# Optimization experiments

Measured on AMD Instinct MI355X. Metric: run time of the kernel, lower is better.

Reference implementation:

```python
import jax, jax.numpy as jnp
import numpy as np

N_NODES = 50000
N_RAND_EDGES = 1_600_000
IN_FEATS = 512
HIDDEN = 256
NUM_CLASSES = 64


def setup_inputs() -> dict:
    key = jax.random.key(0)
    ks = jax.random.split(key, 6)
    src = jax.random.randint(ks[0], (N_RAND_EDGES,), 0, N_NODES, dtype=jnp.int32)
    dst = jax.random.randint(ks[1], (N_RAND_EDGES,), 0, N_NODES, dtype=jnp.int32)
    # dgl.add_self_loop(g): append (i, i) for every node
    loop = jnp.arange(N_NODES, dtype=jnp.int32)
    src = jnp.concatenate([src, loop])
    dst = jnp.concatenate([dst, loop])
    features = jax.random.normal(ks[2], (N_NODES, IN_FEATS), dtype=jnp.float32)
    W_conv = jax.random.normal(ks[3], (IN_FEATS, HIDDEN), dtype=jnp.float32) * (1.0 / np.sqrt(IN_FEATS))
    b_conv = jnp.zeros((HIDDEN,), dtype=jnp.float32)
    W2 = jax.random.normal(ks[4], (HIDDEN, NUM_CLASSES), dtype=jnp.float32) * (1.0 / np.sqrt(HIDDEN))
    b2 = jnp.zeros((NUM_CLASSES,), dtype=jnp.float32)
    return {"features": features, "W_conv": W_conv, "b_conv": b_conv,
            "W2": W2, "b2": b2, "src": src, "dst": dst}


def reference(features, W_conv, b_conv, W2, b2, src, dst):
    N = features.shape[0]
    ones = jnp.ones(src.shape[0], dtype=features.dtype)
    # symmetric ('both') normalization as in DGL GraphConv; self-loops guarantee deg >= 1
    deg_out = jax.ops.segment_sum(ones, src, num_segments=N)
    deg_in = jax.ops.segment_sum(ones, dst, num_segments=N)
    norm_src = jax.lax.rsqrt(deg_out)[:, None]  # [N, 1]
    norm_dst = jax.lax.rsqrt(deg_in)[:, None]
    # in_feats > hidden -> DGL multiplies by the weight before aggregating
    h = (features @ W_conv) * norm_src            # [N, H]
    agg = jax.ops.segment_sum(h[src], dst, num_segments=N)  # sparse SpMM: gather + scatter-add
    x = jax.nn.relu(agg * norm_dst + b_conv)      # [N, H]
    # dropout: identity in eval mode (deterministic reference)
    logits = x @ W2 + b2                          # [N, C]
    return jax.nn.log_softmax(logits, axis=1)
```

## Files before the change

kernel.cpp:

```cpp
#include <hip/hip_runtime.h>

typedef unsigned short u16;
typedef unsigned int u32;
typedef __attribute__((ext_vector_type(4))) float f32x4;
typedef __attribute__((ext_vector_type(8))) short s16x8;
typedef __attribute__((ext_vector_type(4))) unsigned short u16x4;
typedef __attribute__((ext_vector_type(8))) unsigned short u16x8;

#define IN_FEATS 512
#define HIDDEN   256
#define NCLS     64
#define NB       128
#define QBINS    12500
#define EPT      13

#define H8_CLIP  2.5f
#define H8_INV   (127.0f / H8_CLIP)
#define H8_SCALE (H8_CLIP / 127.0f)

static __device__ inline u16 f2bf(float f) {
    unsigned int u = __builtin_bit_cast(unsigned int, f);
    unsigned int r = (u + 0x7FFFu + ((u >> 16) & 1u)) >> 16;
    return (u16)r;
}
static __device__ inline float bf2f(u16 u) {
    unsigned int x = ((unsigned int)u) << 16;
    return __builtin_bit_cast(float, x);
}


__launch_bounds__(1024)
__global__ void khist(const int* __restrict__ src, const int* __restrict__ dst,
                      u16* __restrict__ P, int E, int N) {
    __shared__ int bins[QBINS];
    const int b = blockIdx.x;
    const int t = threadIdx.x;
    const int lo = (int)((long)b * E / NB);
    const int hi = (int)((long)(b + 1) * E / NB);

    int se[EPT], de[EPT];
#pragma unroll
    for (int p = 0; p < EPT; p++) {
        int e = lo + t + p * 1024;
        se[p] = 0; de[p] = 0;
        if (e < hi) { se[p] = src[e]; de[p] = dst[e]; }
    }

#pragma unroll 1
    for (int q = 0; q < 4; q++) {
        const int base = q * QBINS;
        __syncthreads();
        for (int j = t; j < QBINS; j += 1024) bins[j] = 0;
        __syncthreads();
#pragma unroll
        for (int p = 0; p < EPT; p++) {
            int e = lo + t + p * 1024;
            if (e < hi) {
                unsigned rs = (unsigned)(se[p] - base), rd = (unsigned)(de[p] - base);
                if (rs < (unsigned)QBINS) atomicAdd(&bins[rs], 1);
                if (rd < (unsigned)QBINS) atomicAdd(&bins[rd], 0x10000);
            }
        }
        for (int e = lo + t + EPT * 1024; e < hi; e += 1024) {
            int s = src[e], d = dst[e];
            unsigned rs = (unsigned)(s - base), rd = (unsigned)(d - base);
            if (rs < (unsigned)QBINS) atomicAdd(&bins[rs], 1);
            if (rd < (unsigned)QBINS) atomicAdd(&bins[rd], 0x10000);
        }
        __syncthreads();
        for (int j = t; j < QBINS; j += 1024) {
            u32 v = (u32)bins[j];
            P[(size_t)b * 50000 + base + j] = (u16)((v & 0xffu) | ((v >> 8) & 0xff00u));
        }
    }
}

__global__ void kred(u16* __restrict__ P, int* __restrict__ deg_in,
                     float* __restrict__ ns, float* __restrict__ nd, int N) {
    int j = blockIdx.x * blockDim.x + threadIdx.x;
    if (j >= N) return;
    u32 so = 0, si = 0;
#pragma unroll 4
    for (int b = 0; b < NB; b++) {
        u32 v = P[(size_t)b * 50000 + j];
        P[(size_t)b * 50000 + j] = (u16)si;
        so += v & 0xffu;
        si += v >> 8;
    }
    deg_in[j] = (int)si;
    ns[j] = rsqrtf((float)so);
    nd[j] = rsqrtf((float)si);
}

__launch_bounds__(256)
__global__ void kscanA(const int* __restrict__ deg, int* __restrict__ rowptr,
                       int* __restrict__ bsum, int N) {
    __shared__ int wsum[4];
    const int b = blockIdx.x, t = threadIdx.x;
    const int lane = t & 63, wave = t >> 6;
    const int j = b * 256 + t;
    int v = (j < N) ? deg[j] : 0;
    int s = v;
#pragma unroll
    for (int off = 1; off < 64; off <<= 1) {
        int u = __shfl_up(s, off);
        if (lane >= off) s += u;
    }
    if (lane == 63) wsum[wave] = s;
    __syncthreads();
    int woff = 0;
#pragma unroll
    for (int w = 0; w < 4; w++) woff += (w < wave) ? wsum[w] : 0;
    if (j < N) rowptr[j] = woff + s - v;
    if (t == 255) bsum[b] = woff + s;
}

__launch_bounds__(256)
__global__ void kscanB(int* __restrict__ rowptr, const int* __restrict__ bsum,
                       int N, int nblk, int E) {
    __shared__ int wsum[4];
    const int b = blockIdx.x, t = threadIdx.x;
    const int lane = t & 63, wave = t >> 6;
    int v = (t < b && t < nblk) ? bsum[t] : 0;
#pragma unroll
    for (int off = 32; off; off >>= 1) v += __shfl_xor(v, off);
    if (lane == 0) wsum[wave] = v;
    __syncthreads();
    int offsum = wsum[0] + wsum[1] + wsum[2] + wsum[3];
    int j = b * 256 + t;
    if (j < N) rowptr[j] += offsum;
    if (b == 0 && t == 0) rowptr[N] = E;
}

__launch_bounds__(1024)
__global__ void kscat(const int* __restrict__ src, const int* __restrict__ dst,
                      const int* __restrict__ rowptr, const u16* __restrict__ P,
                      int* __restrict__ csc, int E, int N) {
    __shared__ int cur[QBINS];
    const int b = blockIdx.x;
    const int t = threadIdx.x;
    const int lo = (int)((long)b * E / NB);
    const int hi = (int)((long)(b + 1) * E / NB);

    int se[EPT], de[EPT];
#pragma unroll
    for (int p = 0; p < EPT; p++) {
        int e = lo + t + p * 1024;
        se[p] = 0; de[p] = 0;
        if (e < hi) { se[p] = src[e]; de[p] = dst[e]; }
    }

#pragma unroll 1
    for (int q = 0; q < 4; q++) {
        const int base = q * QBINS;
        __syncthreads();
        for (int j = t; j < QBINS; j += 1024) {
            int node = base + j;
            cur[j] = (node < N) ? rowptr[node] + (int)P[(size_t)b * 50000 + node] : 0;
        }
        __syncthreads();
#pragma unroll
        for (int p = 0; p < EPT; p++) {
            int e = lo + t + p * 1024;
            if (e < hi) {
                unsigned rd = (unsigned)(de[p] - base);
                if (rd < (unsigned)QBINS) {
                    int pos = atomicAdd(&cur[rd], 1);
                    csc[pos] = se[p] << 8;
                }
            }
        }
        for (int e = lo + t + EPT * 1024; e < hi; e += 1024) {
            int d = dst[e];
            unsigned rd = (unsigned)(d - base);
            if (rd < (unsigned)QBINS) {
                int pos = atomicAdd(&cur[rd], 1);
                csc[pos] = src[e] << 8;
            }
        }
    }
}


__global__ void k_wt(const float* __restrict__ W, u16* __restrict__ Wt) {
    int i = blockIdx.x * blockDim.x + threadIdx.x;
    if (i < IN_FEATS * HIDDEN) {
        int k = i >> 8, n = i & 255;
        Wt[n * IN_FEATS + k] = f2bf(W[i]);
    }
}

__global__ void k_w2t(const float* __restrict__ W2, u16* __restrict__ W2t) {
    int i = blockIdx.x * blockDim.x + threadIdx.x;
    if (i < HIDDEN * NCLS) {
        int k = i >> 6, n = i & 63;
        W2t[n * HIDDEN + k] = f2bf(W2[i]);
    }
}

__global__ void k_zrow(signed char* __restrict__ h8, int N) {
    ((int*)(h8 + (size_t)N * HIDDEN))[threadIdx.x] = 0;
}


static __device__ inline s16x8 ld_frag(const u16* p) {
    u16x4 lo = *(const u16x4*)p;
    u16x4 hi = *(const u16x4*)(p + 4);
    s16x8 r;
    r[0] = (short)lo.x; r[1] = (short)lo.y; r[2] = (short)lo.z; r[3] = (short)lo.w;
    r[4] = (short)hi.x; r[5] = (short)hi.y; r[6] = (short)hi.z; r[7] = (short)hi.w;
    return r;
}

__launch_bounds__(512)
__global__ void k_gemm1(const float* __restrict__ feat, const u16* __restrict__ Wt,
                        const float* __restrict__ norm_src, signed char* __restrict__ h8, int N) {
    __shared__ __align__(16) u16 At[128][40];
    __shared__ __align__(16) u16 Bt[256][40];
    const int t = threadIdx.x;
    const int lane = t & 63;
    const int wave = t >> 6;
    const int wm = wave & 1;
    const int wn = wave >> 1;
    const int m0 = blockIdx.x * 128;
    const int l15 = lane & 15;
    const int l4 = lane >> 4;

    f32x4 acc[4][4] = {};

    for (int kk = 0; kk < IN_FEATS; kk += 32) {
        __syncthreads();
#pragma unroll
        for (int rnd = 0; rnd < 2; rnd++) {
            int slot = t + rnd * 512;
            int r = slot >> 3, q = slot & 7;
            int gr = m0 + r;
            float4 v = make_float4(0.f, 0.f, 0.f, 0.f);
            if (gr < N) v = *(const float4*)&feat[(size_t)gr * IN_FEATS + kk + q * 4];
            u16x4 p;
            p.x = f2bf(v.x); p.y = f2bf(v.y); p.z = f2bf(v.z); p.w = f2bf(v.w);
            *(u16x4*)&At[r][q * 4] = p;
        }
#pragma unroll
        for (int rnd = 0; rnd < 2; rnd++) {
            int slot = t + rnd * 512;
            int r = slot >> 2, q = slot & 3;
            u16x4 w0 = *(const u16x4*)&Wt[(size_t)r * IN_FEATS + kk + q * 8];
            u16x4 w1 = *(const u16x4*)&Wt[(size_t)r * IN_FEATS + kk + q * 8 + 4];
            *(u16x4*)&Bt[r][q * 8] = w0;
            *(u16x4*)&Bt[r][q * 8 + 4] = w1;
        }
        __syncthreads();

        s16x8 a[4], b[4];
#pragma unroll
        for (int mi = 0; mi < 4; mi++) a[mi] = ld_frag(&At[wm * 64 + mi * 16 + l15][l4 * 8]);
#pragma unroll
        for (int ni = 0; ni < 4; ni++) b[ni] = ld_frag(&Bt[wn * 64 + ni * 16 + l15][l4 * 8]);
#pragma unroll
        for (int mi = 0; mi < 4; mi++)
#pragma unroll
            for (int ni = 0; ni < 4; ni++)
                acc[mi][ni] = __builtin_amdgcn_mfma_f32_16x16x32_bf16(a[mi], b[ni], acc[mi][ni], 0, 0, 0);
    }

#pragma unroll
    for (int mi = 0; mi < 4; mi++) {
#pragma unroll
        for (int q = 0; q < 4; q++) {
            int row = m0 + wm * 64 + mi * 16 + l4 * 4 + q;
            if (row < N) {
                float nsv = norm_src[row] * H8_INV;
#pragma unroll
                for (int ni = 0; ni < 4; ni++) {
                    int col = wn * 64 + ni * 16 + l15;
                    int v = (int)rintf(acc[mi][ni][q] * nsv);
                    v = max(-127, min(127, v));
                    h8[(size_t)row * HIDDEN + col] = (signed char)v;
                }
            }
        }
    }
}

__launch_bounds__(256)
__global__ void k_spmm(const signed char* __restrict__ h8, const int* __restrict__ rowptr,
                       const int* __restrict__ csc, const float* __restrict__ nd,
                       const float* __restrict__ bconv, u16* __restrict__ x, int N) {
    const int t = threadIdx.x;
    const int lane = t & 63;
    const int half = lane >> 5;
    const int hl = lane & 31;
    const int ZOFF = N * HIDDEN;
    const int gw = (blockIdx.x * blockDim.x + t) >> 6;
    const int nw = (gridDim.x * blockDim.x) >> 6;
    const int npair = (N + 1) >> 1;

    for (int pair = gw; pair < npair; pair += nw) {
        int node = pair * 2 + half;
        bool valid = node < N;
        int start = 0, deg = 0;
        if (valid) { start = rowptr[node]; deg = rowptr[node + 1] - start; }
        int maxdeg = max(deg, __shfl_xor(deg, 32));
        int a0 = 0, a1 = 0, a2 = 0, a3 = 0, a4 = 0, a5 = 0, a6 = 0, a7 = 0;

        for (int base = 0; base < maxdeg; base += 32) {
            int ev = ZOFF;
            if (base + hl < deg) ev = csc[start + base + hl];
            int cntmax = min(32, maxdeg - base);
            int i = 0;
            for (; i + 4 <= cntmax; i += 4) {
                int sb = (half << 5) + i;
                int o0 = __shfl(ev, sb);
                int o1 = __shfl(ev, sb + 1);
                int o2 = __shfl(ev, sb + 2);
                int o3 = __shfl(ev, sb + 3);
                int2 w0 = *(const int2*)&h8[o0 + hl * 8];
                int2 w1 = *(const int2*)&h8[o1 + hl * 8];
                int2 w2 = *(const int2*)&h8[o2 + hl * 8];
                int2 w3 = *(const int2*)&h8[o3 + hl * 8];
                a0 += ((w0.x << 24) >> 24) + ((w1.x << 24) >> 24) + ((w2.x << 24) >> 24) + ((w3.x << 24) >> 24);
                a1 += ((w0.x << 16) >> 24) + ((w1.x << 16) >> 24) + ((w2.x << 16) >> 24) + ((w3.x << 16) >> 24);
                a2 += ((w0.x << 8) >> 24) + ((w1.x << 8) >> 24) + ((w2.x << 8) >> 24) + ((w3.x << 8) >> 24);
                a3 += (w0.x >> 24) + (w1.x >> 24) + (w2.x >> 24) + (w3.x >> 24);
                a4 += ((w0.y << 24) >> 24) + ((w1.y << 24) >> 24) + ((w2.y << 24) >> 24) + ((w3.y << 24) >> 24);
                a5 += ((w0.y << 16) >> 24) + ((w1.y << 16) >> 24) + ((w2.y << 16) >> 24) + ((w3.y << 16) >> 24);
                a6 += ((w0.y << 8) >> 24) + ((w1.y << 8) >> 24) + ((w2.y << 8) >> 24) + ((w3.y << 8) >> 24);
                a7 += (w0.y >> 24) + (w1.y >> 24) + (w2.y >> 24) + (w3.y >> 24);
            }
            for (; i < cntmax; i++) {
                int o = __shfl(ev, (half << 5) + i);
                int2 w = *(const int2*)&h8[o + hl * 8];
                a0 += (w.x << 24) >> 24;
                a1 += (w.x << 16) >> 24;
                a2 += (w.x << 8) >> 24;
                a3 += w.x >> 24;
                a4 += (w.y << 24) >> 24;
                a5 += (w.y << 16) >> 24;
                a6 += (w.y << 8) >> 24;
                a7 += w.y >> 24;
            }
        }

        if (valid) {
            float scnd = nd[node] * H8_SCALE;
            float4 ba = *(const float4*)&bconv[hl * 8];
            float4 bb = *(const float4*)&bconv[hl * 8 + 4];
            u16x8 o;
            o[0] = f2bf(fmaxf((float)a0 * scnd + ba.x, 0.f));
            o[1] = f2bf(fmaxf((float)a1 * scnd + ba.y, 0.f));
            o[2] = f2bf(fmaxf((float)a2 * scnd + ba.z, 0.f));
            o[3] = f2bf(fmaxf((float)a3 * scnd + ba.w, 0.f));
            o[4] = f2bf(fmaxf((float)a4 * scnd + bb.x, 0.f));
            o[5] = f2bf(fmaxf((float)a5 * scnd + bb.y, 0.f));
            o[6] = f2bf(fmaxf((float)a6 * scnd + bb.z, 0.f));
            o[7] = f2bf(fmaxf((float)a7 * scnd + bb.w, 0.f));
            *(u16x8*)&x[(size_t)node * HIDDEN + hl * 8] = o;
        }
    }
}

__launch_bounds__(256)
__global__ void k_gemm2(const u16* __restrict__ x, const u16* __restrict__ W2t,
                        const float* __restrict__ b2, float* __restrict__ out, int N) {
    __shared__ __align__(16) u16 Bs[NCLS][HIDDEN + 8];
    const int t = threadIdx.x;
    for (int i = t; i < NCLS * HIDDEN / 8; i += 256) {
        int idx = i * 8;
        int n = idx >> 8, k = idx & 255;
        *(u16x8*)&Bs[n][k] = *(const u16x8*)&W2t[n * HIDDEN + k];
    }
    __syncthreads();

    const int lane = t & 63;
    const int wave = t >> 6;
    const int l15 = lane & 15;
    const int l4 = lane >> 4;
    const int r0 = blockIdx.x * 128 + wave * 32;

    float bb[4];
#pragma unroll
    for (int ni = 0; ni < 4; ni++) bb[ni] = b2[ni * 16 + l15];

    f32x4 acc[2][4] = {};
#pragma unroll
    for (int kk = 0; kk < HIDDEN; kk += 32) {
        s16x8 b[4];
#pragma unroll
        for (int ni = 0; ni < 4; ni++) b[ni] = ld_frag(&Bs[ni * 16 + l15][kk + l4 * 8]);
#pragma unroll
        for (int mi = 0; mi < 2; mi++) {
            int row = r0 + mi * 16 + l15;
            s16x8 a = {};
            if (row < N) a = ld_frag(&x[(size_t)row * HIDDEN + kk + l4 * 8]);
#pragma unroll
            for (int ni = 0; ni < 4; ni++)
                acc[mi][ni] = __builtin_amdgcn_mfma_f32_16x16x32_bf16(a, b[ni], acc[mi][ni], 0, 0, 0);
        }
    }

#pragma unroll
    for (int mi = 0; mi < 2; mi++) {
#pragma unroll
        for (int q = 0; q < 4; q++) {
            int row = r0 + mi * 16 + l4 * 4 + q;
            float v0 = acc[mi][0][q] + bb[0];
            float v1 = acc[mi][1][q] + bb[1];
            float v2 = acc[mi][2][q] + bb[2];
            float v3 = acc[mi][3][q] + bb[3];
            float m = fmaxf(fmaxf(v0, v1), fmaxf(v2, v3));
#pragma unroll
            for (int off = 1; off < 16; off <<= 1) m = fmaxf(m, __shfl_xor(m, off));
            float s = __expf(v0 - m) + __expf(v1 - m) + __expf(v2 - m) + __expf(v3 - m);
#pragma unroll
            for (int off = 1; off < 16; off <<= 1) s += __shfl_xor(s, off);
            float lg = m + __logf(s);
            if (row < N) {
                out[(size_t)row * NCLS + 0 * 16 + l15] = v0 - lg;
                out[(size_t)row * NCLS + 1 * 16 + l15] = v1 - lg;
                out[(size_t)row * NCLS + 2 * 16 + l15] = v2 - lg;
                out[(size_t)row * NCLS + 3 * 16 + l15] = v3 - lg;
            }
        }
    }
}


extern "C" void kernel_launch(void* const* d_in, const int* in_sizes, int n_in,
                              void* d_out, int out_size, void* d_ws, size_t ws_size,
                              hipStream_t stream) {
    const float* feat = (const float*)d_in[0];
    const float* Wc   = (const float*)d_in[1];
    const float* bc   = (const float*)d_in[2];
    const float* W2   = (const float*)d_in[3];
    const float* b2   = (const float*)d_in[4];
    const int*   src  = (const int*)d_in[5];
    const int*   dst  = (const int*)d_in[6];
    const int N = in_sizes[0] / IN_FEATS;
    const int E = in_sizes[5];
    float* out = (float*)d_out;

    char* ws = (char*)d_ws;
    size_t off = 0;
    auto alloc = [&](size_t b) {
        char* p = ws + off;
        off = (off + b + 255) & ~(size_t)255;
        return p;
    };
    signed char* h8 = (signed char*)alloc((size_t)(N + 1) * HIDDEN);
    u16* x      = (u16*)alloc((size_t)N * HIDDEN * 2);
    u16* Wt     = (u16*)alloc((size_t)IN_FEATS * HIDDEN * 2);
    u16* W2t    = (u16*)alloc((size_t)HIDDEN * NCLS * 2);
    int* deg_in = (int*)alloc((size_t)N * 4);
    int* rowptr = (int*)alloc((size_t)(N + 1) * 4);
    int* bsum   = (int*)alloc((size_t)256 * 4);
    float* ns   = (float*)alloc((size_t)N * 4);
    float* nd   = (float*)alloc((size_t)N * 4);
    int* csc    = (int*)alloc((size_t)E * 4);
    u16* P      = (u16*)alloc((size_t)NB * 50000 * 2);

    const int nblk = (N + 255) / 256;

    khist<<<dim3(NB), dim3(1024), 0, stream>>>(src, dst, P, E, N);
    kred<<<dim3((N + 255) / 256), dim3(256), 0, stream>>>(P, deg_in, ns, nd, N);
    kscanA<<<dim3(nblk), dim3(256), 0, stream>>>(deg_in, rowptr, bsum, N);
    kscanB<<<dim3(nblk), dim3(256), 0, stream>>>(rowptr, bsum, N, nblk, E);
    kscat<<<dim3(NB), dim3(1024), 0, stream>>>(src, dst, rowptr, P, csc, E, N);
    k_wt<<<dim3((IN_FEATS * HIDDEN + 255) / 256), dim3(256), 0, stream>>>(Wc, Wt);
    k_w2t<<<dim3((HIDDEN * NCLS + 255) / 256), dim3(256), 0, stream>>>(W2, W2t);
    k_zrow<<<dim3(1), dim3(64), 0, stream>>>(h8, N);
    k_gemm1<<<dim3((N + 127) / 128), dim3(512), 0, stream>>>(feat, Wt, ns, h8, N);
    k_spmm<<<dim3(2048), dim3(256), 0, stream>>>(h8, rowptr, csc, nd, bc, x, N);
    k_gemm2<<<dim3((N + 127) / 128), dim3(256), 0, stream>>>(x, W2t, b2, out, N);
}
```

Before: 172.9 us.

## Fuse degree reduction into scan, merge prep kernels, load GEMM1 weights directly

Merges the per-node degree reduction into the first scan kernel, so the deg_in array and one launch go away. Combines the two weight-transpose kernels and the zero-row kernel into one prep launch. In GEMM1, the B fragments are now read straight from global/L2 memory instead of being staged through shared memory, which frees LDS and removes the staging stores. The trade-off is more uncoalesced global reads of Wt per wave, with no data reuse across waves through LDS.

New measurement: 180.9 us. 4.7% more time.

```diff
diff --git a/kernel.cpp b/kernel.cpp
--- a/kernel.cpp
+++ b/kernel.cpp
@@ -22,10 +22,6 @@
     unsigned int u = __builtin_bit_cast(unsigned int, f);
     unsigned int r = (u + 0x7FFFu + ((u >> 16) & 1u)) >> 16;
     return (u16)r;
-}
-static __device__ inline float bf2f(u16 u) {
-    unsigned int x = ((unsigned int)u) << 16;
-    return __builtin_bit_cast(float, x);
 }
 
 
@@ -75,31 +71,27 @@
     }
 }
 
-__global__ void kred(u16* __restrict__ P, int* __restrict__ deg_in,
-                     float* __restrict__ ns, float* __restrict__ nd, int N) {
-    int j = blockIdx.x * blockDim.x + threadIdx.x;
-    if (j >= N) return;
-    u32 so = 0, si = 0;
-#pragma unroll 4
-    for (int b = 0; b < NB; b++) {
-        u32 v = P[(size_t)b * 50000 + j];
-        P[(size_t)b * 50000 + j] = (u16)si;
-        so += v & 0xffu;
-        si += v >> 8;
-    }
-    deg_in[j] = (int)si;
-    ns[j] = rsqrtf((float)so);
-    nd[j] = rsqrtf((float)si);
-}
-
 __launch_bounds__(256)
-__global__ void kscanA(const int* __restrict__ deg, int* __restrict__ rowptr,
-                       int* __restrict__ bsum, int N) {
+__global__ void kredscan(u16* __restrict__ P, int* __restrict__ rowptr,
+                         int* __restrict__ bsum, float* __restrict__ ns,
+                         float* __restrict__ nd, int N) {
     __shared__ int wsum[4];
     const int b = blockIdx.x, t = threadIdx.x;
     const int lane = t & 63, wave = t >> 6;
     const int j = b * 256 + t;
-    int v = (j < N) ? deg[j] : 0;
+    u32 so = 0, si = 0;
+    if (j < N) {
+#pragma unroll 8
+        for (int bb = 0; bb < NB; bb++) {
+            u32 v = P[(size_t)bb * 50000 + j];
+            P[(size_t)bb * 50000 + j] = (u16)si;
+            so += v & 0xffu;
+            si += v >> 8;
+        }
+        ns[j] = rsqrtf((float)so);
+        nd[j] = rsqrtf((float)si);
+    }
+    int v = (j < N) ? (int)si : 0;
     int s = v;
 #pragma unroll
     for (int off = 1; off < 64; off <<= 1) {
@@ -181,25 +173,21 @@
     }
 }
 
-
-__global__ void k_wt(const float* __restrict__ W, u16* __restrict__ Wt) {
+__global__ void kprep(const float* __restrict__ W, u16* __restrict__ Wt,
+                      const float* __restrict__ W2, u16* __restrict__ W2t,
+                      signed char* __restrict__ h8, int N) {
     int i = blockIdx.x * blockDim.x + threadIdx.x;
     if (i < IN_FEATS * HIDDEN) {
         int k = i >> 8, n = i & 255;
         Wt[n * IN_FEATS + k] = f2bf(W[i]);
-    }
-}
-
-__global__ void k_w2t(const float* __restrict__ W2, u16* __restrict__ W2t) {
-    int i = blockIdx.x * blockDim.x + threadIdx.x;
-    if (i < HIDDEN * NCLS) {
-        int k = i >> 6, n = i & 63;
-        W2t[n * HIDDEN + k] = f2bf(W2[i]);
-    }
-}
-
-__global__ void k_zrow(signed char* __restrict__ h8, int N) {
-    ((int*)(h8 + (size_t)N * HIDDEN))[threadIdx.x] = 0;
+    } else if (i < IN_FEATS * HIDDEN + HIDDEN * NCLS) {
+        int ii = i - IN_FEATS * HIDDEN;
+        int k = ii >> 6, n = ii & 63;
+        W2t[n * HIDDEN + k] = f2bf(W2[ii]);
+    } else if (i < IN_FEATS * HIDDEN + HIDDEN * NCLS + 64) {
+        int ii = i - IN_FEATS * HIDDEN - HIDDEN * NCLS;
+        ((int*)(h8 + (size_t)N * HIDDEN))[ii] = 0;
+    }
 }
 
 
@@ -216,7 +204,6 @@
 __global__ void k_gemm1(const float* __restrict__ feat, const u16* __restrict__ Wt,
                         const float* __restrict__ norm_src, signed char* __restrict__ h8, int N) {
     __shared__ __align__(16) u16 At[128][40];
-    __shared__ __align__(16) u16 Bt[256][40];
     const int t = threadIdx.x;
     const int lane = t & 63;
     const int wave = t >> 6;
@@ -241,22 +228,14 @@
             p.x = f2bf(v.x); p.y = f2bf(v.y); p.z = f2bf(v.z); p.w = f2bf(v.w);
             *(u16x4*)&At[r][q * 4] = p;
         }
-#pragma unroll
-        for (int rnd = 0; rnd < 2; rnd++) {
-            int slot = t + rnd * 512;
-            int r = slot >> 2, q = slot & 3;
-            u16x4 w0 = *(const u16x4*)&Wt[(size_t)r * IN_FEATS + kk + q * 8];
-            u16x4 w1 = *(const u16x4*)&Wt[(size_t)r * IN_FEATS + kk + q * 8 + 4];
-            *(u16x4*)&Bt[r][q * 8] = w0;
-            *(u16x4*)&Bt[r][q * 8 + 4] = w1;
-        }
         __syncthreads();
 
         s16x8 a[4], b[4];
 #pragma unroll
+        for (int ni = 0; ni < 4; ni++)
+            b[ni] = ld_frag(&Wt[(size_t)(wn * 64 + ni * 16 + l15) * IN_FEATS + kk + l4 * 8]);
+#pragma unroll
         for (int mi = 0; mi < 4; mi++) a[mi] = ld_frag(&At[wm * 64 + mi * 16 + l15][l4 * 8]);
-#pragma unroll
-        for (int ni = 0; ni < 4; ni++) b[ni] = ld_frag(&Bt[wn * 64 + ni * 16 + l15][l4 * 8]);
 #pragma unroll
         for (int mi = 0; mi < 4; mi++)
 #pragma unroll
@@ -451,7 +430,6 @@
     u16* x      = (u16*)alloc((size_t)N * HIDDEN * 2);
     u16* Wt     = (u16*)alloc((size_t)IN_FEATS * HIDDEN * 2);
     u16* W2t    = (u16*)alloc((size_t)HIDDEN * NCLS * 2);
-    int* deg_in = (int*)alloc((size_t)N * 4);
     int* rowptr = (int*)alloc((size_t)(N + 1) * 4);
     int* bsum   = (int*)alloc((size_t)256 * 4);
     float* ns   = (float*)alloc((size_t)N * 4);
@@ -460,15 +438,13 @@
     u16* P      = (u16*)alloc((size_t)NB * 50000 * 2);
 
     const int nblk = (N + 255) / 256;
+    const int nprep = (IN_FEATS * HIDDEN + HIDDEN * NCLS + 64 + 255) / 256;
 
     khist<<<dim3(NB), dim3(1024), 0, stream>>>(src, dst, P, E, N);
-    kred<<<dim3((N + 255) / 256), dim3(256), 0, stream>>>(P, deg_in, ns, nd, N);
-    kscanA<<<dim3(nblk), dim3(256), 0, stream>>>(deg_in, rowptr, bsum, N);
+    kredscan<<<dim3(nblk), dim3(256), 0, stream>>>(P, rowptr, bsum, ns, nd, N);
     kscanB<<<dim3(nblk), dim3(256), 0, stream>>>(rowptr, bsum, N, nblk, E);
     kscat<<<dim3(NB), dim3(1024), 0, stream>>>(src, dst, rowptr, P, csc, E, N);
-    k_wt<<<dim3((IN_FEATS * HIDDEN + 255) / 256), dim3(256), 0, stream>>>(Wc, Wt);
-    k_w2t<<<dim3((HIDDEN * NCLS + 255) / 256), dim3(256), 0, stream>>>(W2, W2t);
-    k_zrow<<<dim3(1), dim3(64), 0, stream>>>(h8, N);
+    kprep<<<dim3(nprep), dim3(256), 0, stream>>>(Wc, Wt, W2, W2t, h8, N);
     k_gemm1<<<dim3((N + 127) / 128), dim3(512), 0, stream>>>(feat, Wt, ns, h8, N);
     k_spmm<<<dim3(2048), dim3(256), 0, stream>>>(h8, rowptr, csc, nd, bc, x, N);
     k_gemm2<<<dim3((N + 127) / 128), dim3(256), 0, stream>>>(x, W2t, b2, out, N);
```
